# Kernel tuning notes

Measured on AMD Instinct MI355X. Metric: run time of the kernel, lower is better.

Reference implementation:

```python
import jax, jax.numpy as jnp
import numpy as np

EPS = 1e-5
NEG_SLOPE = 0.2  # DGL GATConv default leaky_relu slope


def conv1d_same(x, w, b):
    # x: [N, Cin, T], w: [Cout, Cin, K]
    y = jax.lax.conv_general_dilated(x, w, (1,), 'SAME',
                                     dimension_numbers=('NCW', 'OIW', 'NCW'))
    return y + b[None, :, None]


def gated_conv(x, w1, b1, w2, b2, w3, b3):
    # Temporal_Gated_Conv: relu(conv1(x)*sigmoid(conv2(x)) + conv3(x))
    return jax.nn.relu(conv1d_same(x, w1, b1) * jax.nn.sigmoid(conv1d_same(x, w2, b2))
                       + conv1d_same(x, w3, b3))


def bn3(x, g, b):
    # BatchNorm1d on [N, C, T]: stats over (N, T), training mode (batch stats)
    m = jnp.mean(x, (0, 2), keepdims=True)
    v = jnp.var(x, (0, 2), keepdims=True)
    return (x - m) * jax.lax.rsqrt(v + EPS) * g[None, :, None] + b[None, :, None]


def bn2(x, g, b):
    # BatchNorm1d on [N, F]: stats over N
    m = jnp.mean(x, 0, keepdims=True)
    v = jnp.var(x, 0, keepdims=True)
    return (x - m) * jax.lax.rsqrt(v + EPS) * g[None, :] + b[None, :]


def setup_inputs() -> dict:
    key = jax.random.key(0)
    ks = jax.random.split(key, 24)
    N, C, T, H, DEG = 20000, 32, 8, 4, 16
    F = C * T          # GAT in/out feats per head = 256
    E = N * DEG
    s = 0.05
    inp = {
        'X': jax.random.normal(ks[0], (N, C, T), jnp.float32),
        'src': jax.random.randint(ks[1], (E,), 0, N, jnp.int32),
        'dst': jax.random.randint(ks[2], (E,), 0, N, jnp.int32),
        # residual_proj: Conv1d(C->C, k=1)
        'rp_w': jax.random.normal(ks[3], (C, C, 1), jnp.float32) * s,
        'rp_b': jnp.zeros((C,), jnp.float32),
        # gated_conv1: three Conv1d(C->C, k=3)
        'g1_w1': jax.random.normal(ks[4], (C, C, 3), jnp.float32) * s,
        'g1_b1': jnp.zeros((C,), jnp.float32),
        'g1_w2': jax.random.normal(ks[5], (C, C, 3), jnp.float32) * s,
        'g1_b2': jnp.zeros((C,), jnp.float32),
        'g1_w3': jax.random.normal(ks[6], (C, C, 3), jnp.float32) * s,
        'g1_b3': jnp.zeros((C,), jnp.float32),
        'bn0_g': jnp.ones((C,), jnp.float32),
        'bn0_b': jnp.zeros((C,), jnp.float32),
        # GATConv: fc [H*F, F], attn_l/attn_r [H, F], bias [H*F]
        'gat_w': jax.random.normal(ks[7], (H * F, F), jnp.float32) * s,
        'attn_l': jax.random.normal(ks[8], (H, F), jnp.float32) * s,
        'attn_r': jax.random.normal(ks[9], (H, F), jnp.float32) * s,
        'gat_bias': jnp.zeros((H * F,), jnp.float32),
        'bn1_g': jnp.ones((H * F,), jnp.float32),
        'bn1_b': jnp.zeros((H * F,), jnp.float32),
        # gated_conv2: three Conv1d(C*H -> C, k=3)
        'g2_w1': jax.random.normal(ks[10], (C, C * H, 3), jnp.float32) * s,
        'g2_b1': jnp.zeros((C,), jnp.float32),
        'g2_w2': jax.random.normal(ks[11], (C, C * H, 3), jnp.float32) * s,
        'g2_b2': jnp.zeros((C,), jnp.float32),
        'g2_w3': jax.random.normal(ks[12], (C, C * H, 3), jnp.float32) * s,
        'g2_b3': jnp.zeros((C,), jnp.float32),
        'bn2_g': jnp.ones((C,), jnp.float32),
        'bn2_b': jnp.zeros((C,), jnp.float32),
    }
    return inp


def reference(X, src, dst, rp_w, rp_b, g1_w1, g1_b1, g1_w2, g1_b2, g1_w3, g1_b3,
              bn0_g, bn0_b, gat_w, attn_l, attn_r, gat_bias, bn1_g, bn1_b,
              g2_w1, g2_b1, g2_w2, g2_b2, g2_w3, g2_b3, bn2_g, bn2_b):
    N, C, T = X.shape
    H, F = attn_l.shape

    residual = conv1d_same(X, rp_w, rp_b)                      # [N, C, T]
    x = gated_conv(X, g1_w1, g1_b1, g1_w2, g1_b2, g1_w3, g1_b3)
    x = bn3(x, bn0_g, bn0_b)
    x = x.reshape(N, C * T)                                    # row-major flatten == torch .view

    # --- DGL GATConv (feat_drop=attn_drop=0, concat heads, ReLU activation) ---
    h = (x @ gat_w.T).reshape(N, H, F)                         # fc projection
    el = jnp.sum(h * attn_l, -1)                               # [N, H]
    er = jnp.sum(h * attn_r, -1)                               # [N, H]
    e = jax.nn.leaky_relu(el[src] + er[dst], NEG_SLOPE)        # [E, H]
    # segment softmax over incoming edges of each dst node
    m = jax.ops.segment_max(e, dst, num_segments=N)            # [N, H]
    ee = jnp.exp(e - m[dst])
    den = jax.ops.segment_sum(ee, dst, num_segments=N)         # [N, H]
    alpha = ee / den[dst]                                      # [E, H]
    rst = jax.ops.segment_sum(alpha[:, :, None] * h[src], dst, num_segments=N)  # [N, H, F]
    rst = jax.nn.relu(rst + gat_bias.reshape(H, F))

    x = rst.reshape(N, H * F)                                  # concat heads
    x = bn2(x, bn1_g, bn1_b)
    x = x.reshape(N, (H * F) // T, T)                          # [N, C*H, T]
    x = gated_conv(x, g2_w1, g2_b1, g2_w2, g2_b2, g2_w3, g2_b3)
    x = bn3(x, bn2_g, bn2_b)
    x = jax.nn.relu(x + residual)                              # self.last=True, dropout=0
    return x
```

## Files before the change

### kernel.cpp

```cpp
#include <hip/hip_runtime.h>
#include <stdint.h>

#define NN 20000
#define NE 320000

typedef unsigned short us16;
typedef __attribute__((ext_vector_type(8))) short short8;
typedef __attribute__((ext_vector_type(4))) float f32x4;

union U4 { uint4 v; us16 s[8]; unsigned u[4]; };
union U2 { uint2 v; us16 s[4]; };

__device__ __forceinline__ float b2f(us16 u){ return __uint_as_float(((unsigned)u)<<16); }
__device__ __forceinline__ us16 f2b(float f){
  unsigned u = __float_as_uint(f);
  u += 0x7fffu + ((u>>16)&1u);
  return (us16)(u>>16);
}

__device__ __forceinline__ void gll16(const void* g, void* l){
  __builtin_amdgcn_global_load_lds((const __attribute__((address_space(1))) void*)g,
                                   (__attribute__((address_space(3))) void*)l, 16, 0, 0);
}

__global__ __launch_bounds__(256) void k_misc(
    const float* __restrict__ gatw, us16* __restrict__ Wb,
    const float* __restrict__ w1, const float* __restrict__ w2, const float* __restrict__ w3,
    us16* __restrict__ Wt,
    const float* __restrict__ c1w1, const float* __restrict__ c1w2, const float* __restrict__ c1w3,
    const float* __restrict__ rp_w, us16* __restrict__ Wt1,
    const float* __restrict__ attnl, const float* __restrict__ attnr,
    float* __restrict__ wl, float* __restrict__ wr,
    const int* __restrict__ dst, int* __restrict__ counts)
{
  const int b = blockIdx.x, tid = threadIdx.x;
  if(b < 256){
    int i = b*256 + tid;
    float4 v = *(const float4*)(gatw + (size_t)i*4);
    U2 o;
    o.s[0]=f2b(v.x); o.s[1]=f2b(v.y); o.s[2]=f2b(v.z); o.s[3]=f2b(v.w);
    *(uint2*)(Wb + (size_t)i*4) = o.v;
  } else if(b < 400){
    int i = (b-256)*256 + tid;
    int s = i/12288, rem = i%12288;
    int co3 = rem>>7, ci = rem&127;
    const float* w = (co3<32) ? w1 : (co3<64) ? w2 : w3;
    Wt[i] = f2b(w[(co3&31)*384 + ci*3 + s]);
  } else if(b < 448){
    int i = (b-400)*256 + tid;
    int s = i>>12, rem = i&4095;
    int co3 = rem>>5, ci = rem&31;
    float v;
    if(co3 < 96){
      const float* w = (co3<32) ? c1w1 : (co3<64) ? c1w2 : c1w3;
      v = w[(co3&31)*96 + ci*3 + s];
    } else {
      v = (s==1) ? rp_w[(co3-96)*32 + ci] : 0.f;
    }
    Wt1[i] = f2b(v);
  } else if(b < 480){
    int bb = b-448;
    int sel = bb>>4, hd = (bb>>2)&3, fq = bb&3;
    const float* attn = sel ? attnr : attnl;
    int k = tid;
    float s = 0.f;
    int f0 = fq*64;
    #pragma unroll 8
    for(int f=f0; f<f0+64; f++)
      s = fmaf(attn[hd*256+f], gatw[(size_t)(hd*256+f)*256 + k], s);
    atomicAdd(&((sel ? wr : wl)[hd*256+k]), s);
  } else {
    int e = (b-480)*256 + tid;
    if(e < NE) atomicAdd(&counts[dst[e]], 1);
  }
}

__global__ __launch_bounds__(256) void k_gemm1(
    const float* __restrict__ X, const us16* __restrict__ Wt1,
    const float* __restrict__ b1, const float* __restrict__ b2, const float* __restrict__ b3,
    const float* __restrict__ rp_b,
    us16* __restrict__ gc1, us16* __restrict__ resid,
    float* __restrict__ bn0_sum, float* __restrict__ bn0_sq,
    const int* __restrict__ counts, int* __restrict__ offsets, int* __restrict__ cursor)
{
  __shared__ float smemF[5760];
  __shared__ float redS[32], redQ[32];
  __shared__ int wred[4];
  const int tid = threadIdx.x;
  if(blockIdx.x < 1250){
    us16* As = (us16*)smemF;
    us16* Bs = As + 6400;
    if(tid<32){ redS[tid]=0.f; redQ[tid]=0.f; }
    const int node0 = blockIdx.x*16;
    const int lane = tid&63, wv = tid>>6;
    const int mrow = lane&15, kg = (lane>>4)*8;
    for(int idx=tid; idx<1024; idx+=256){
      int n = idx>>6, rem = idx&63, slot = (rem>>5)*9, ci = rem&31;
      As[n*400 + slot*40 + ci] = 0;
    }
    #pragma unroll
    for(int i=0;i<4;i++){
      int idx = i*256 + tid;
      int n = idx>>6, rem = idx&63, ci = rem>>1, tq = rem&1;
      float4 xv = *(const float4*)(X + (size_t)(node0+n)*256 + ci*8 + tq*4);
      us16* p = &As[n*400 + (tq*4+1)*40 + ci];
      p[0]   = f2b(xv.x);
      p[40]  = f2b(xv.y);
      p[80]  = f2b(xv.z);
      p[120] = f2b(xv.w);
    }
    f32x4 acc[2][8] = {};
    for(int s=0; s<3; s++){
      if(s) __syncthreads();
      #pragma unroll
      for(int i=0;i<2;i++){
        int c = i*256 + tid;
        int co = c>>2, cq = c&3;
        *(uint4*)&Bs[co*40 + cq*8] = *(const uint4*)(Wt1 + s*4096 + co*32 + cq*8);
      }
      __syncthreads();
      short8 af[2], bfr[8];
      #pragma unroll
      for(int i=0;i<2;i++){
        int r = wv*32 + i*16 + mrow;
        af[i] = *(const short8*)&As[(r>>3)*400 + ((r&7)+s)*40 + kg];
      }
      #pragma unroll
      for(int j=0;j<8;j++)
        bfr[j] = *(const short8*)&Bs[(j*16 + mrow)*40 + kg];
      #pragma unroll
      for(int i=0;i<2;i++){
        #pragma unroll
        for(int j=0;j<8;j++)
          acc[i][j] = __builtin_amdgcn_mfma_f32_16x16x32_bf16(af[i], bfr[j], acc[i][j], 0, 0, 0);
      }
    }
    __syncthreads();
    us16* Og = (us16*)smemF;
    us16* Or = Og + 4096;
    const int coA = lane&15, coB = coA+16;
    const float b1A=b1[coA], b2A=b2[coA], b3A=b3[coA], brA=rp_b[coA];
    const float b1B=b1[coB], b2B=b2[coB], b3B=b3[coB], brB=rp_b[coB];
    float sA=0.f, qA=0.f, sB=0.f, qB=0.f;
    const int g = lane>>4;
    #pragma unroll
    for(int i=0;i<2;i++){
      int node = wv*4 + i*2 + (g>>1);
      int t0 = (g&1)*4;
      U2 pA, pB, rA2, rB2;
      #pragma unroll
      for(int r=0;r<4;r++){
        float c1 = acc[i][0][r]+b1A, c2 = acc[i][2][r]+b2A, c3 = acc[i][4][r]+b3A;
        float rr = acc[i][6][r]+brA;
        float sg = 1.f/(1.f+__expf(-c2));
        float v = fmaf(c1,sg,c3); v = v>0.f ? v : 0.f;
        sA += v; qA += v*v;
        pA.s[r]=f2b(v); rA2.s[r]=f2b(rr);
        c1 = acc[i][1][r]+b1B; c2 = acc[i][3][r]+b2B; c3 = acc[i][5][r]+b3B;
        rr = acc[i][7][r]+brB;
        sg = 1.f/(1.f+__expf(-c2));
        v = fmaf(c1,sg,c3); v = v>0.f ? v : 0.f;
        sB += v; qB += v*v;
        pB.s[r]=f2b(v); rB2.s[r]=f2b(rr);
      }
      *(uint2*)&Og[node*256 + coA*8 + t0] = pA.v;
      *(uint2*)&Og[node*256 + coB*8 + t0] = pB.v;
      *(uint2*)&Or[node*256 + coA*8 + t0] = rA2.v;
      *(uint2*)&Or[node*256 + coB*8 + t0] = rB2.v;
    }
    sA += __shfl_xor(sA,16,64); sA += __shfl_xor(sA,32,64);
    qA += __shfl_xor(qA,16,64); qA += __shfl_xor(qA,32,64);
    sB += __shfl_xor(sB,16,64); sB += __shfl_xor(sB,32,64);
    qB += __shfl_xor(qB,16,64); qB += __shfl_xor(qB,32,64);
    if(lane < 16){
      atomicAdd(&redS[coA], sA); atomicAdd(&redQ[coA], qA);
      atomicAdd(&redS[coB], sB); atomicAdd(&redQ[coB], qB);
    }
    __syncthreads();
    #pragma unroll
    for(int i=0;i<2;i++){
      int idx = i*256 + tid;
      *(uint4*)(gc1   + (size_t)node0*256 + (size_t)idx*8) = *(const uint4*)&Og[idx*8];
      *(uint4*)(resid + (size_t)node0*256 + (size_t)idx*8) = *(const uint4*)&Or[idx*8];
    }
    if(tid<32)      atomicAdd(&bn0_sum[tid], redS[tid]);
    else if(tid<64) atomicAdd(&bn0_sq[tid-32], redQ[tid-32]);
  } else {
    const int lane = tid&63, wv = tid>>6;
    int running = 0;
    int4 cur;
    {
      int idx = tid*4;
      cur = *(const int4*)(counts + idx);
    }
    for(int t=0; t<20; t++){
      int4 nxt; nxt.x=0; nxt.y=0; nxt.z=0; nxt.w=0;
      if(t < 19){
        int idx = (t+1)*1024 + tid*4;
        if(idx+3 < NN) nxt = *(const int4*)(counts + idx);
        else {
          if(idx   < NN) nxt.x = counts[idx];
          if(idx+1 < NN) nxt.y = counts[idx+1];
          if(idx+2 < NN) nxt.z = counts[idx+2];
          if(idx+3 < NN) nxt.w = counts[idx+3];
        }
      }
      int s = cur.x + cur.y + cur.z + cur.w;
      int incl = s;
      #pragma unroll
      for(int off=1; off<64; off<<=1){
        int v = __shfl_up(incl, off, 64);
        if(lane >= off) incl += v;
      }
      if(lane==63) wred[wv] = incl;
      __syncthreads();
      int woff = 0, btot = 0;
      #pragma unroll
      for(int w2=0; w2<4; w2++){
        int x = wred[w2];
        btot += x;
        if(w2 < wv) woff += x;
      }
      int e0 = running + woff + incl - s;
      int idx = t*1024 + tid*4;
      int4 o; o.x=e0; o.y=e0+cur.x; o.z=o.y+cur.y; o.w=o.z+cur.z;
      if(idx+3 < NN){
        *(int4*)(offsets+idx) = o;
        *(int4*)(cursor+idx)  = o;
      } else {
        if(idx   < NN){ offsets[idx]  =o.x; cursor[idx]  =o.x; }
        if(idx+1 < NN){ offsets[idx+1]=o.y; cursor[idx+1]=o.y; }
        if(idx+2 < NN){ offsets[idx+2]=o.z; cursor[idx+2]=o.z; }
        if(idx+3 < NN){ offsets[idx+3]=o.w; cursor[idx+3]=o.w; }
      }
      running += btot;
      cur = nxt;
      __syncthreads();
    }
    if(tid==0) offsets[NN] = running;
  }
}

__global__ __launch_bounds__(256) void k_eler2(const us16* __restrict__ gc1,
    const float* __restrict__ bn0_sum, const float* __restrict__ bn0_sq,
    const float* __restrict__ bn0g, const float* __restrict__ bn0b,
    const float* __restrict__ wl, const float* __restrict__ wr,
    float* __restrict__ el, float* __restrict__ er)
{
  __shared__ float sa[32], sb[32];
  const int tid = threadIdx.x;
  if(tid<32){
    float m = bn0_sum[tid]*(1.f/160000.f);
    float v = bn0_sq[tid]*(1.f/160000.f) - m*m;
    float a = bn0g[tid]*rsqrtf(v + 1e-5f);
    sa[tid] = a; sb[tid] = bn0b[tid] - m*a;
  }
  __syncthreads();
  const int wv = tid>>6, lane = tid&63;
  const int node = blockIdx.x*4 + wv;
  U2 g; g.v = *(const uint2*)(gc1 + (size_t)node*256 + lane*4);
  const float a = sa[lane>>1], b = sb[lane>>1];
  float xv[4];
  #pragma unroll
  for(int j=0;j<4;j++) xv[j] = fmaf(a, b2f(g.s[j]), b);
  float res[8];
  #pragma unroll
  for(int hd=0; hd<4; hd++){
    float4 lv = *(const float4*)(wl + hd*256 + lane*4);
    float4 rv = *(const float4*)(wr + hd*256 + lane*4);
    res[hd]   = xv[0]*lv.x + xv[1]*lv.y + xv[2]*lv.z + xv[3]*lv.w;
    res[4+hd] = xv[0]*rv.x + xv[1]*rv.y + xv[2]*rv.z + xv[3]*rv.w;
  }
  #pragma unroll
  for(int o=32;o;o>>=1){
    #pragma unroll
    for(int k=0;k<8;k++) res[k] += __shfl_xor(res[k], o, 64);
  }
  if(lane==0){
    #pragma unroll
    for(int hd=0;hd<4;hd++){ el[node*4+hd]=res[hd]; er[node*4+hd]=res[4+hd]; }
  }
}

__global__ __launch_bounds__(256) void k_scatter(const int* __restrict__ src, const int* __restrict__ dst,
    int* __restrict__ cursor, int* __restrict__ esrc,
    const float* __restrict__ el, const float* __restrict__ er,
    float* __restrict__ ew)
{
  int e = blockIdx.x*256 + threadIdx.x;
  if(e < NE){
    int s = src[e], d = dst[e];
    int pos = atomicAdd(&cursor[d], 1);
    esrc[pos] = s;
    float4 lv = *(const float4*)(el + s*4);
    float4 rv = *(const float4*)(er + d*4);
    float4 sc;
    sc.x = lv.x+rv.x; sc.x = sc.x>0.f ? sc.x : 0.2f*sc.x;
    sc.y = lv.y+rv.y; sc.y = sc.y>0.f ? sc.y : 0.2f*sc.y;
    sc.z = lv.z+rv.z; sc.z = sc.z>0.f ? sc.z : 0.2f*sc.z;
    sc.w = lv.w+rv.w; sc.w = sc.w>0.f ? sc.w : 0.2f*sc.w;
    *(float4*)(ew + (size_t)pos*4) = sc;
  }
}

__global__ __launch_bounds__(256) void k_agg2(
    const int* __restrict__ offsets, const int* __restrict__ esrc,
    const float* __restrict__ ew, const us16* __restrict__ gc1,
    const float* __restrict__ bn0_sum, const float* __restrict__ bn0_sq,
    const float* __restrict__ bn0g, const float* __restrict__ bn0b,
    us16* __restrict__ Axg)
{
  const int tid = threadIdx.x;
  const int wv = tid>>6, lane = tid&63;
  const int node = blockIdx.x*4 + wv;
  const int ch = lane>>1;
  float mmn = bn0_sum[ch]*(1.f/160000.f);
  float vvn = bn0_sq[ch]*(1.f/160000.f) - mmn*mmn;
  float sa = bn0g[ch]*rsqrtf(vvn + 1e-5f);
  float sb = bn0b[ch] - mmn*sa;
  const int beg = offsets[node];
  const int deg = offsets[node+1] - beg;
  const int h = lane>>4, i0 = lane&15;
  float m = -3.0e38f;
  for(int i=i0; i<deg; i+=16) m = fmaxf(m, ew[(size_t)(beg+i)*4 + h]);
  m = fmaxf(m, __shfl_xor(m,1,64)); m = fmaxf(m, __shfl_xor(m,2,64));
  m = fmaxf(m, __shfl_xor(m,4,64)); m = fmaxf(m, __shfl_xor(m,8,64));
  float den = 0.f;
  for(int i=i0; i<deg; i+=16) den += __expf(ew[(size_t)(beg+i)*4 + h] - m);
  den += __shfl_xor(den,1,64); den += __shfl_xor(den,2,64);
  den += __shfl_xor(den,4,64); den += __shfl_xor(den,8,64);
  const float m0=__shfl(m,0,64),   m1=__shfl(m,16,64),  m2=__shfl(m,32,64),  m3=__shfl(m,48,64);
  const float d0=__shfl(den,0,64), d1=__shfl(den,16,64),d2=__shfl(den,32,64),d3=__shfl(den,48,64);
  const float v0=d0>0.f?1.f/d0:0.f, v1=d1>0.f?1.f/d1:0.f,
              v2=d2>0.f?1.f/d2:0.f, v3=d3>0.f?1.f/d3:0.f;
  float a0c[4]={},a1c[4]={},a2c[4]={},a3c[4]={};
  #pragma unroll 4
  for(int j=0; j<deg; j++){
    int pos = beg+j;
    float4 w4 = *(const float4*)(ew + (size_t)pos*4);
    int sN = esrc[pos];
    U2 hv; hv.v = *(const uint2*)(gc1 + (size_t)sN*256 + lane*4);
    float e0 = __expf(w4.x-m0)*v0;
    float e1 = __expf(w4.y-m1)*v1;
    float e2 = __expf(w4.z-m2)*v2;
    float e3 = __expf(w4.w-m3)*v3;
    #pragma unroll
    for(int kk=0;kk<4;kk++){
      float x = b2f(hv.s[kk]);
      a0c[kk] = fmaf(e0,x,a0c[kk]);
      a1c[kk] = fmaf(e1,x,a1c[kk]);
      a2c[kk] = fmaf(e2,x,a2c[kk]);
      a3c[kk] = fmaf(e3,x,a3c[kk]);
    }
  }
  const float sbi = sb * ((deg>0)?1.f:0.f);
  U2 o0,o1,o2,o3;
  #pragma unroll
  for(int kk=0;kk<4;kk++){
    o0.s[kk]=f2b(fmaf(sa,a0c[kk],sbi));
    o1.s[kk]=f2b(fmaf(sa,a1c[kk],sbi));
    o2.s[kk]=f2b(fmaf(sa,a2c[kk],sbi));
    o3.s[kk]=f2b(fmaf(sa,a3c[kk],sbi));
  }
  *(uint2*)(Axg + ((size_t)node)*256            + lane*4) = o0.v;
  *(uint2*)(Axg + ((size_t)NN + node)*256       + lane*4) = o1.v;
  *(uint2*)(Axg + ((size_t)2*NN + node)*256     + lane*4) = o2.v;
  *(uint2*)(Axg + ((size_t)3*NN + node)*256     + lane*4) = o3.v;
}

__global__ __launch_bounds__(512) void k_gemm3(const us16* __restrict__ Axg, const us16* __restrict__ Wb,
    const float* __restrict__ gbias, us16* __restrict__ rst,
    float* __restrict__ bn1_sum, float* __restrict__ bn1_sq)
{
  __shared__ us16 sm[17408];
  us16* As = sm;
  us16* Bs = sm + 4096;
  const int tid = threadIdx.x;
  const int row0 = blockIdx.x*128;
  const int hd   = blockIdx.y;
  const us16* A  = Axg + (size_t)hd*NN*256;
  const us16* Bf = Wb  + (size_t)hd*256*256;
  const int lane = tid&63, wv = tid>>6;
  const int wm = wv&1, wn = wv>>1;
  const int mrow = lane&15, g4 = lane>>4;
  const us16* sgA; const us16* sgB[2];
  us16 *sdA, *sdB[2];
  {
    int r = wv*16 + (lane>>2);
    int c = (lane&3) ^ (r&3);
    int ga = row0 + r; if(ga >= NN) ga = NN-1;
    sgA = A + (size_t)ga*256 + c*8;
    sdA = As + wv*512;
    #pragma unroll
    for(int i=0;i<2;i++){
      int rb = wv*32 + i*16 + (lane>>2);
      int cbk = (lane&3) ^ (rb&3);
      sgB[i] = Bf + (size_t)rb*256 + cbk*8;
      sdB[i] = Bs + wv*1024 + i*512;
    }
  }
  f32x4 acc[4][4] = {};
  for(int k0=0; k0<256; k0+=32){
    if(k0) __syncthreads();
    gll16(sgA + k0, sdA);
    gll16(sgB[0] + k0, sdB[0]);
    gll16(sgB[1] + k0, sdB[1]);
    __syncthreads();
    short8 af[4], bfr[4];
    #pragma unroll
    for(int i=0;i<4;i++){
      int r = wm*64 + i*16 + mrow;
      af[i] = *(const short8*)&As[r*32 + ((g4 ^ (r&3))<<3)];
    }
    #pragma unroll
    for(int j=0;j<4;j++){
      int r = wn*64 + j*16 + mrow;
      bfr[j] = *(const short8*)&Bs[r*32 + ((g4 ^ (r&3))<<3)];
    }
    #pragma unroll
    for(int i=0;i<4;i++){
      #pragma unroll
      for(int j=0;j<4;j++)
        acc[i][j] = __builtin_amdgcn_mfma_f32_16x16x32_bf16(af[i], bfr[j], acc[i][j], 0, 0, 0);
    }
  }
  float gb[4];
  #pragma unroll
  for(int j=0;j<4;j++)
    gb[j] = gbias[hd*256 + wn*64 + j*16 + (lane&15)];
  us16* Og = sm;
  #pragma unroll
  for(int p=0; p<2; p++){
    __syncthreads();
    if((wn>>1) == p){
      float cs[4]={}, cq[4]={};
      #pragma unroll
      for(int i=0;i<4;i++){
        #pragma unroll
        for(int j=0;j<4;j++){
          #pragma unroll
          for(int r=0;r<4;r++){
            int rl = wm*64 + i*16 + (lane>>4)*4 + r;
            float v = acc[i][j][r] + gb[j];
            v = v>0.f ? v : 0.f;
            Og[rl*136 + (wn&1)*64 + j*16 + (lane&15)] = f2b(v);
            if(row0 + rl < NN){ cs[j] += v; cq[j] += v*v; }
          }
        }
      }
      #pragma unroll
      for(int j=0;j<4;j++){
        cs[j] += __shfl_xor(cs[j],16,64); cs[j] += __shfl_xor(cs[j],32,64);
        cq[j] += __shfl_xor(cq[j],16,64); cq[j] += __shfl_xor(cq[j],32,64);
      }
      if(lane < 16){
        #pragma unroll
        for(int j=0;j<4;j++){
          int col = hd*256 + p*128 + (wn&1)*64 + j*16 + lane;
          atomicAdd(&bn1_sum[col], cs[j]);
          atomicAdd(&bn1_sq[col],  cq[j]);
        }
      }
    }
    __syncthreads();
    #pragma unroll
    for(int i=0;i<4;i++){
      int idx = i*512 + tid;
      int rowl = idx>>4, cq2 = idx&15;
      int g = row0 + rowl;
      if(g < NN)
        *(uint4*)(rst + (size_t)g*1024 + hd*256 + p*128 + cq2*8) = *(const uint4*)&Og[rowl*136 + cq2*8];
    }
  }
}

__global__ __launch_bounds__(256) void k_gemm2(
    const us16* __restrict__ rst, const us16* __restrict__ Wt,
    const float* __restrict__ bn1_sum, const float* __restrict__ bn1_sq,
    const float* __restrict__ bn1g, const float* __restrict__ bn1b,
    const float* __restrict__ b1, const float* __restrict__ b2, const float* __restrict__ b3,
    us16* __restrict__ y2, float* __restrict__ bn2_sum, float* __restrict__ bn2_sq)
{
  __shared__ us16 As[11520];
  __shared__ us16 Bs[6144];
  __shared__ float redS[32], redQ[32];
  const int tid = threadIdx.x;
  if(tid<32){ redS[tid]=0.f; redQ[tid]=0.f; }
  const int node0 = blockIdx.x*16;
  const int lane = tid&63, wv = tid>>6;
  const int mrow = lane&15, kg = (lane>>4)*8, g4 = lane>>4;
  const int csrc = (lane&7) ^ (lane>>3);
  const int brow_off = (lane>>3)*128 + csrc*8;
  us16* bdst[3];
  const us16* bsrc[3];
  #pragma unroll
  for(int i=0;i<3;i++){
    bdst[i] = Bs + (i*4+wv)*512;
    bsrc[i] = Wt + (size_t)(i*4+wv)*8*128 + brow_off;
  }
  for(int idx=tid; idx<2048; idx+=256){
    int n = idx>>7, rem = idx&127, slot = (rem>>6)*9, ci = rem&63;
    As[n*720 + slot*72 + ci] = 0;
  }
  f32x4 acc[2][6] = {};
  for(int kc=0; kc<2; kc++){
    float ra[8], rb[8];
    {
      int f0 = (kc*64 + (tid&63))*8;
      float4 s0 = *(const float4*)(bn1_sum + f0), s1 = *(const float4*)(bn1_sum + f0 + 4);
      float4 q0 = *(const float4*)(bn1_sq  + f0), q1 = *(const float4*)(bn1_sq  + f0 + 4);
      float4 g0 = *(const float4*)(bn1g    + f0), g1 = *(const float4*)(bn1g    + f0 + 4);
      float4 h0 = *(const float4*)(bn1b    + f0), h1 = *(const float4*)(bn1b    + f0 + 4);
      const float* sp = (const float*)&s0; const float* qp = (const float*)&q0;
      const float* gp = (const float*)&g0; const float* hp = (const float*)&h0;
      #pragma unroll
      for(int t=0;t<8;t++){
        float sv = (t<4)? sp[t] : ((const float*)&s1)[t-4];
        float qv = (t<4)? qp[t] : ((const float*)&q1)[t-4];
        float gv = (t<4)? gp[t] : ((const float*)&g1)[t-4];
        float hv = (t<4)? hp[t] : ((const float*)&h1)[t-4];
        float m = sv*(1.f/20000.f);
        float v = qv*(1.f/20000.f) - m*m;
        float a = gv*rsqrtf(v + 1e-5f);
        ra[t] = a; rb[t] = hv - m*a;
      }
    }
    if(kc) __syncthreads();
    #pragma unroll
    for(int i=0;i<4;i++){
      int idx = i*256 + tid;
      int n = idx>>6, cil = idx&63;
      int ci = kc*64 + cil;
      U4 in; in.v = *(const uint4*)(rst + (size_t)(node0+n)*1024 + ci*8);
      us16* p = &As[n*720 + 72 + cil];
      #pragma unroll
      for(int t=0;t<8;t++)
        p[t*72] = f2b(fmaf(ra[t], b2f(in.s[t]), rb[t]));
    }
    for(int s=0; s<3; s++){
      if(s) __syncthreads();
      #pragma unroll
      for(int i=0;i<3;i++)
        gll16(bsrc[i] + s*12288 + kc*64, bdst[i]);
      __syncthreads();
      #pragma unroll
      for(int kk=0; kk<64; kk+=32){
        short8 af[2], bfr[6];
        #pragma unroll
        for(int i=0;i<2;i++){
          int r = wv*32 + i*16 + mrow;
          af[i] = *(const short8*)&As[(r>>3)*720 + ((r&7)+s)*72 + kk + kg];
        }
        #pragma unroll
        for(int j=0;j<6;j++){
          int r = j*16 + mrow;
          int q = (kk>>3) + g4;
          bfr[j] = *(const short8*)&Bs[r*64 + ((q ^ (r&7))<<3)];
        }
        #pragma unroll
        for(int i=0;i<2;i++){
          #pragma unroll
          for(int j=0;j<6;j++)
            acc[i][j] = __builtin_amdgcn_mfma_f32_16x16x32_bf16(af[i], bfr[j], acc[i][j], 0, 0, 0);
        }
      }
    }
  }
  __syncthreads();
  us16* Og = (us16*)As;
  const int coA = lane&15, coB = coA+16;
  const float b1A=b1[coA], b2A=b2[coA], b3A=b3[coA];
  const float b1B=b1[coB], b2B=b2[coB], b3B=b3[coB];
  float sA=0.f, qA=0.f, sB=0.f, qB=0.f;
  const int g = lane>>4;
  #pragma unroll
  for(int i=0;i<2;i++){
    int node = wv*4 + i*2 + (g>>1);
    int t0 = (g&1)*4;
    U2 pA, pB;
    #pragma unroll
    for(int r=0;r<4;r++){
      float c1 = acc[i][0][r]+b1A, c2 = acc[i][2][r]+b2A, c3 = acc[i][4][r]+b3A;
      float sg = 1.f/(1.f+__expf(-c2));
      float v = fmaf(c1,sg,c3); v = v>0.f ? v : 0.f;
      sA += v; qA += v*v; pA.s[r]=f2b(v);
      c1 = acc[i][1][r]+b1B; c2 = acc[i][3][r]+b2B; c3 = acc[i][5][r]+b3B;
      sg = 1.f/(1.f+__expf(-c2));
      v = fmaf(c1,sg,c3); v = v>0.f ? v : 0.f;
      sB += v; qB += v*v; pB.s[r]=f2b(v);
    }
    *(uint2*)&Og[node*256 + coA*8 + t0] = pA.v;
    *(uint2*)&Og[node*256 + coB*8 + t0] = pB.v;
  }
  sA += __shfl_xor(sA,16,64); sA += __shfl_xor(sA,32,64);
  qA += __shfl_xor(qA,16,64); qA += __shfl_xor(qA,32,64);
  sB += __shfl_xor(sB,16,64); sB += __shfl_xor(sB,32,64);
  qB += __shfl_xor(qB,16,64); qB += __shfl_xor(qB,32,64);
  if(lane < 16){
    atomicAdd(&redS[coA], sA); atomicAdd(&redQ[coA], qA);
    atomicAdd(&redS[coB], sB); atomicAdd(&redQ[coB], qB);
  }
  __syncthreads();
  #pragma unroll
  for(int i=0;i<2;i++){
    int idx = i*256 + tid;
    *(uint4*)(y2 + (size_t)node0*256 + (size_t)idx*8) = *(const uint4*)&Og[idx*8];
  }
  if(tid<32)      atomicAdd(&bn2_sum[tid], redS[tid]);
  else if(tid<64) atomicAdd(&bn2_sq[tid-32], redQ[tid-32]);
}

__global__ __launch_bounds__(256) void k_final(const us16* __restrict__ y2,
    const float* __restrict__ bn2_sum, const float* __restrict__ bn2_sq,
    const float* __restrict__ bn2g, const float* __restrict__ bn2b,
    const us16* __restrict__ resid, float* __restrict__ out)
{
  __shared__ float fa[32], fb[32];
  const int tid = threadIdx.x;
  if(tid<32){
    float m = bn2_sum[tid]*(1.f/160000.f);
    float v = bn2_sq[tid]*(1.f/160000.f) - m*m;
    float a = bn2g[tid]*rsqrtf(v + 1e-5f);
    fa[tid] = a; fb[tid] = bn2b[tid] - m*a;
  }
  __syncthreads();
  size_t base = ((size_t)blockIdx.x*256 + tid)*8;
  int ch = (int)((base>>3)&31);
  float a = fa[ch], b = fb[ch];
  U4 yv, rv;
  yv.v = *(const uint4*)(y2+base);
  rv.v = *(const uint4*)(resid+base);
  float4 o0, o1;
  float vv[8];
  #pragma unroll
  for(int j=0;j<8;j++){
    float v = fmaf(a, b2f(yv.s[j]), b) + b2f(rv.s[j]);
    vv[j] = v>0.f ? v : 0.f;
  }
  o0.x=vv[0]; o0.y=vv[1]; o0.z=vv[2]; o0.w=vv[3];
  o1.x=vv[4]; o1.y=vv[5]; o1.z=vv[6]; o1.w=vv[7];
  *(float4*)(out+base)   = o0;
  *(float4*)(out+base+4) = o1;
}

extern "C" void kernel_launch(void* const* d_in, const int* in_sizes, int n_in,
                              void* d_out, int out_size, void* d_ws, size_t ws_size,
                              hipStream_t stream)
{
  const float* X    = (const float*)d_in[0];
  const int*  src   = (const int*)d_in[1];
  const int*  dst   = (const int*)d_in[2];
  const float* rp_w = (const float*)d_in[3];
  const float* rp_b = (const float*)d_in[4];
  const float* g1w1 = (const float*)d_in[5];
  const float* g1b1 = (const float*)d_in[6];
  const float* g1w2 = (const float*)d_in[7];
  const float* g1b2 = (const float*)d_in[8];
  const float* g1w3 = (const float*)d_in[9];
  const float* g1b3 = (const float*)d_in[10];
  const float* bn0g = (const float*)d_in[11];
  const float* bn0b = (const float*)d_in[12];
  const float* gatw = (const float*)d_in[13];
  const float* attnl= (const float*)d_in[14];
  const float* attnr= (const float*)d_in[15];
  const float* gbias= (const float*)d_in[16];
  const float* bn1g = (const float*)d_in[17];
  const float* bn1b = (const float*)d_in[18];
  const float* g2w1 = (const float*)d_in[19];
  const float* g2b1 = (const float*)d_in[20];
  const float* g2w2 = (const float*)d_in[21];
  const float* g2b2 = (const float*)d_in[22];
  const float* g2w3 = (const float*)d_in[23];
  const float* g2b3 = (const float*)d_in[24];
  const float* bn2g = (const float*)d_in[25];
  const float* bn2b = (const float*)d_in[26];
  float* out = (float*)d_out;
  (void)in_sizes; (void)n_in; (void)out_size; (void)ws_size;

  char* w = (char*)d_ws;
  float* bn0_sum = (float*)w;
  float* bn0_sq  = bn0_sum + 32;
  float* bn1_sum = bn0_sum + 64;
  float* bn1_sq  = bn1_sum + 1024;
  float* bn2_sum = bn1_sq  + 1024;
  float* bn2_sq  = bn2_sum + 32;
  float* wl      = bn2_sq + 32;
  float* wr      = wl + 1024;
  int*   counts  = (int*)(wr + 1024);
  size_t zeroBytes = (size_t)((char*)(counts + NN) - w);
  int*   offsets = counts + NN;
  int*   cursor  = offsets + 20004;
  int*   esrc    = cursor + NN;
  float* el      = (float*)(esrc + NE);
  float* er      = el + NN*4;
  float* ew      = er + NN*4;
  us16*  wb      = (us16*)(ew + (size_t)NE*4);
  us16*  resid   = wb + 262144;
  us16*  gc1     = resid + 5120000;
  us16*  Axg     = gc1   + 5120000;
  us16*  rst     = Axg   + 20480000;
  us16*  Wt      = rst   + 20480000;
  us16*  Wt1     = Wt    + 36864;
  us16*  y2      = gc1;

  hipMemsetAsync(d_ws, 0, zeroBytes, stream);
  k_misc<<<1730, 256, 0, stream>>>(gatw, wb, g2w1, g2w2, g2w3, Wt,
                                   g1w1, g1w2, g1w3, rp_w, Wt1,
                                   attnl, attnr, wl, wr, dst, counts);
  k_gemm1<<<1251, 256, 0, stream>>>(X, Wt1, g1b1, g1b2, g1b3, rp_b,
                                    gc1, resid, bn0_sum, bn0_sq,
                                    counts, offsets, cursor);
  k_eler2<<<5000, 256, 0, stream>>>(gc1, bn0_sum, bn0_sq, bn0g, bn0b, wl, wr, el, er);
  k_scatter<<<1250, 256, 0, stream>>>(src, dst, cursor, esrc, el, er, ew);
  k_agg2<<<5000, 256, 0, stream>>>(offsets, esrc, ew, gc1, bn0_sum, bn0_sq, bn0g, bn0b, Axg);
  k_gemm3<<<dim3(157, 4), 512, 0, stream>>>(Axg, wb, gbias, rst, bn1_sum, bn1_sq);
  k_gemm2<<<1250, 256, 0, stream>>>(rst, Wt, bn1_sum, bn1_sq, bn1g, bn1b,
                                    g2b1, g2b2, g2b3, y2, bn2_sum, bn2_sq);
  k_final<<<2500, 256, 0, stream>>>(y2, bn2_sum, bn2_sq, bn2g, bn2b, resid, out);
}
```

Before: 351.1 us.

## Double-buffer LDS tiles in k_gemm3 with async prefetch two steps ahead

Splits the GEMM's shared memory into two A/B buffers. Global-to-LDS loads for K-step it+2 are issued while step it computes, with s_waitcnt vmcnt and raw s_barrier replacing the per-iteration __syncthreads pairs. The aim is to hide global load latency behind MFMA work. In exchange, LDS use grows, which may lower occupancy, and correctness now depends on the manual vmcnt accounting.

```diff
diff --git a/kernel.cpp b/kernel.cpp
--- a/kernel.cpp
+++ b/kernel.cpp
@@ -372,9 +372,7 @@
     const float* __restrict__ gbias, us16* __restrict__ rst,
     float* __restrict__ bn1_sum, float* __restrict__ bn1_sq)
 {
-  __shared__ us16 sm[17408];
-  us16* As = sm;
-  us16* Bs = sm + 4096;
+  __shared__ us16 sm[24576];
   const int tid = threadIdx.x;
   const int row0 = blockIdx.x*128;
   const int hd   = blockIdx.y;
@@ -390,38 +388,51 @@
     int c = (lane&3) ^ (r&3);
     int ga = row0 + r; if(ga >= NN) ga = NN-1;
     sgA = A + (size_t)ga*256 + c*8;
-    sdA = As + wv*512;
+    sdA = sm + wv*512;
     #pragma unroll
     for(int i=0;i<2;i++){
       int rb = wv*32 + i*16 + (lane>>2);
       int cbk = (lane&3) ^ (rb&3);
       sgB[i] = Bf + (size_t)rb*256 + cbk*8;
-      sdB[i] = Bs + wv*1024 + i*512;
-    }
-  }
+      sdB[i] = sm + 8192 + wv*1024 + i*512;
+    }
+  }
+  gll16(sgA,        sdA);
+  gll16(sgB[0],     sdB[0]);
+  gll16(sgB[1],     sdB[1]);
+  gll16(sgA + 32,   sdA + 4096);
+  gll16(sgB[0] + 32, sdB[0] + 8192);
+  gll16(sgB[1] + 32, sdB[1] + 8192);
   f32x4 acc[4][4] = {};
-  for(int k0=0; k0<256; k0+=32){
-    if(k0) __syncthreads();
-    gll16(sgA + k0, sdA);
-    gll16(sgB[0] + k0, sdB[0]);
-    gll16(sgB[1] + k0, sdB[1]);
-    __syncthreads();
+  for(int it=0; it<8; ++it){
+    if(it < 7) asm volatile("s_waitcnt vmcnt(3)" ::: "memory");
+    else       asm volatile("s_waitcnt vmcnt(0)" ::: "memory");
+    __builtin_amdgcn_s_barrier();
+    const us16* Ac = sm + (it&1)*4096;
+    const us16* Bc = sm + 8192 + (it&1)*8192;
     short8 af[4], bfr[4];
     #pragma unroll
     for(int i=0;i<4;i++){
       int r = wm*64 + i*16 + mrow;
-      af[i] = *(const short8*)&As[r*32 + ((g4 ^ (r&3))<<3)];
+      af[i] = *(const short8*)&Ac[r*32 + ((g4 ^ (r&3))<<3)];
     }
     #pragma unroll
     for(int j=0;j<4;j++){
       int r = wn*64 + j*16 + mrow;
-      bfr[j] = *(const short8*)&Bs[r*32 + ((g4 ^ (r&3))<<3)];
+      bfr[j] = *(const short8*)&Bc[r*32 + ((g4 ^ (r&3))<<3)];
     }
     #pragma unroll
     for(int i=0;i<4;i++){
       #pragma unroll
       for(int j=0;j<4;j++)
         acc[i][j] = __builtin_amdgcn_mfma_f32_16x16x32_bf16(af[i], bfr[j], acc[i][j], 0, 0, 0);
+    }
+    __builtin_amdgcn_s_barrier();
+    if(it < 6){
+      int k0 = (it+2)*32;
+      gll16(sgA + k0,    sdA + (it&1)*4096);
+      gll16(sgB[0] + k0, sdB[0] + (it&1)*8192);
+      gll16(sgB[1] + k0, sdB[1] + (it&1)*8192);
     }
   }
   float gb[4];
```

After: 336.3 us, median of 2. 4.2% less time.
